# Kernel tuning notes

Measured on AMD Instinct MI355X. Metric: run time of the kernel, lower is better.

Reference implementation:

```python
import jax, jax.numpy as jnp
import numpy as np

N_ITER = 3
N_CLASS = 10
N_ROUTE = 1152  # 32*6*6

def _conv(x, w, b, stride):
    y = jax.lax.conv_general_dilated(x, w, window_strides=(stride, stride), padding='VALID',
                                     dimension_numbers=('NCHW', 'OIHW', 'NCHW'))
    return y + b[None, :, None, None]

def setup_inputs() -> dict:
    key = jax.random.key(0)
    ks = jax.random.split(key, 7)
    B = 256
    return {
        'x': jax.random.normal(ks[0], (B, 1, 28, 28), jnp.float32),
        'conv1_w': jax.random.normal(ks[1], (256, 1, 9, 9), jnp.float32) * 0.05,
        'conv1_b': jax.random.normal(ks[2], (256,), jnp.float32) * 0.05,
        'conv2_w': jax.random.normal(ks[3], (256, 256, 9, 9), jnp.float32) * 0.02,
        'conv2_b': jax.random.normal(ks[4], (256,), jnp.float32) * 0.02,
        'W': jax.random.normal(ks[5], (10, 32, 6, 6, 16, 8), jnp.float32) * 0.1,
        'Wb': jax.random.normal(ks[6], (10, 32, 6, 6, 16), jnp.float32) * 0.1,
    }

def reference(x, conv1_w, conv1_b, conv2_w, conv2_b, W, Wb):
    # conv1 (no activation, matching the original forward)
    h = _conv(x, conv1_w, conv1_b, 1)                 # [B,256,20,20]
    prim = _conv(h, conv2_w, conv2_b, 2)              # [B,256,6,6]
    prim = prim.reshape(-1, 32, 6, 6, 8)              # same raw .view as torch
    # fused per-location linear: u_hat[b,j,k,l,i,o]
    u_hat = jnp.einsum('bjklc,ijkloc->bjklio', prim, W) + Wb.transpose(1, 2, 3, 0, 4)[None]
    B = u_hat.shape[0]
    xr = u_hat.reshape(B, N_CLASS, N_ROUTE, 16)       # same raw .view as torch
    bij = jnp.zeros((N_CLASS, N_ROUTE), u_hat.dtype)
    v = None
    for r in range(N_ITER):
        c = jax.nn.softmax(bij, axis=1)               # [10,1152]
        v = jnp.einsum('in,bink->bik', c, xr)         # [B,10,16]
        # squash over the whole [B,16] tensor per class i (as in original x.norm())
        nrm = jnp.sqrt(jnp.sum(v * v, axis=(0, 2), keepdims=True))
        n2 = nrm * nrm
        v = (n2 / (1.0 + n2)) * (v / nrm)
        if r < N_ITER - 1:
            bij = bij + jnp.einsum('bink,bik->in', xr, v)
    # torch.stack(outputs) -> [10,B,16], then .view(-1,10,16)
    return jnp.transpose(v, (1, 0, 2)).reshape(-1, N_CLASS, 16)
```

## Files before the change

kernel.cpp:

```cpp
#include <hip/hip_runtime.h>
#include <hip/hip_bf16.h>

#define DI __device__ __forceinline__

typedef unsigned int u32;
typedef unsigned short u16;
typedef __attribute__((ext_vector_type(8))) short short8;
typedef __attribute__((ext_vector_type(4))) float f32x4;

DI u16 f2bf(float f) {
  union { float f; u32 x; } t; t.f = f;
  u32 x = t.x;
  u32 r = (x + 0x7fffu + ((x >> 16) & 1u)) >> 16;
  return (u16)r;
}

typedef __attribute__((address_space(3))) u32 lds_u32;
typedef const __attribute__((address_space(1))) u32 gbl_u32;
DI void gl_lds16(const u16* g, u16* l) {
  __builtin_amdgcn_global_load_lds((gbl_u32*)(const void*)g, (lds_u32*)(void*)l, 16, 0, 0);
}

__global__ __launch_bounds__(256) void pre_kernel(
    const float* __restrict__ x, const float* __restrict__ w1,
    const float* __restrict__ b1, const float* __restrict__ w2,
    u16* __restrict__ hT, u16* __restrict__ w2bT) {
  __shared__ union {
    struct { float xs[784]; u16 im[400 * 96]; u16 ws[256 * 96]; } c1;
    float w2s[5184];
  } S;
  int tid = threadIdx.x;
  if (blockIdx.x >= 256) {
    int oc = blockIdx.x - 256;
    for (int ch = 0; ch < 4; ++ch) {
      __syncthreads();
      for (int t = tid; t < 5184; t += 256) S.w2s[t] = w2[(size_t)oc * 20736 + ch * 5184 + t];
      __syncthreads();
      for (int t = tid; t < 5184; t += 256) {
        int tap = t >> 6, icl = t & 63;
        w2bT[((size_t)tap * 256 + oc) * 256 + ch * 64 + icl] = f2bf(S.w2s[icl * 81 + tap]);
      }
    }
    return;
  }
  int b = blockIdx.x;
  int lane = tid & 63, wid = tid >> 6;
  const float* xb = x + (size_t)b * 784;
  for (int t = tid; t < 784; t += 256) S.c1.xs[t] = xb[t];
  for (int t = tid; t < 20736; t += 256) {
    int oc = t / 81, kk = t % 81;
    int g = (kk >> 3) & 3, ph = (kk & ~31) | (((g ^ ((oc >> 1) & 3)) << 3)) | (kk & 7);
    S.c1.ws[oc * 96 + ph] = f2bf(w1[t]);
  }
  for (int t = tid; t < 256 * 15; t += 256) {
    int oc = t / 15, kk = 81 + t % 15;
    int g = (kk >> 3) & 3, ph = (kk & ~31) | (((g ^ ((oc >> 1) & 3)) << 3)) | (kk & 7);
    S.c1.ws[oc * 96 + ph] = 0;
  }
  __syncthreads();
  for (int t = tid; t < 32400; t += 256) {
    int pix = t / 81, kk = t % 81;
    int py = pix / 20, px = pix % 20, ky = kk / 9, kx = kk % 9;
    int g = (kk >> 3) & 3, ph = (kk & ~31) | (((g ^ ((pix >> 1) & 3)) << 3)) | (kk & 7);
    S.c1.im[pix * 96 + ph] = f2bf(S.c1.xs[(py + ky) * 28 + px + kx]);
  }
  for (int t = tid; t < 400 * 15; t += 256) {
    int pix = t / 15, kk = 81 + t % 15;
    int g = (kk >> 3) & 3, ph = (kk & ~31) | (((g ^ ((pix >> 1) & 3)) << 3)) | (kk & 7);
    S.c1.im[pix * 96 + ph] = 0;
  }
  __syncthreads();
  int l15 = lane & 15, lh = lane >> 4;
  int slot8 = (lh ^ ((l15 >> 1) & 3)) << 3;
  short8 br[4][3];
  float bias[4];
#pragma unroll
  for (int ni = 0; ni < 4; ++ni) {
    int row = wid * 64 + ni * 16 + l15;
    bias[ni] = b1[row];
#pragma unroll
    for (int ksb = 0; ksb < 3; ++ksb)
      br[ni][ksb] = *(const short8*)&S.c1.ws[row * 96 + ksb * 32 + slot8];
  }
  for (int mt = 0; mt < 25; ++mt) {
    f32x4 acc[4];
#pragma unroll
    for (int ni = 0; ni < 4; ++ni) acc[ni] = (f32x4){0.f, 0.f, 0.f, 0.f};
    short8 ar[3];
#pragma unroll
    for (int ksb = 0; ksb < 3; ++ksb)
      ar[ksb] = *(const short8*)&S.c1.im[(mt * 16 + l15) * 96 + ksb * 32 + slot8];
#pragma unroll
    for (int ksb = 0; ksb < 3; ++ksb)
#pragma unroll
      for (int ni = 0; ni < 4; ++ni)
        acc[ni] = __builtin_amdgcn_mfma_f32_16x16x32_bf16(ar[ksb], br[ni][ksb], acc[ni], 0, 0, 0);
#pragma unroll
    for (int ni = 0; ni < 4; ++ni)
#pragma unroll
      for (int reg = 0; reg < 4; ++reg)
        hT[((size_t)b * 400 + mt * 16 + lh * 4 + reg) * 256 + wid * 64 + ni * 16 + l15] =
            f2bf(acc[ni][reg] + bias[ni]);
  }
}

__global__ __launch_bounds__(512, 2) void conv2_mfma_kernel(
    const u16* __restrict__ hT, const u16* __restrict__ w2bT,
    float* __restrict__ pp) {
  __shared__ u16 Ab[2][16384];
  __shared__ u16 Bb[2][16384];
  int bid = blockIdx.x;
  int xcd = bid & 7, rank = bid >> 3;
  int work = (xcd < 4 ? xcd * 32 : 128 + (xcd - 4) * 31) + rank;
  int ks = work / 36, p = work % 36;
  int py = p / 6, px = p % 6;
  int tid = threadIdx.x, wid = tid >> 6, lane = tid & 63;
  int ntap = (ks < 4) ? 12 : 11;
  int nch = ntap * 4;

  const u16* srcA[4];
  const u16* srcB[4];
#pragma unroll
  for (int c = 0; c < 4; ++c) {
    int row = wid * 32 + c * 8 + (lane >> 3);
    int gsw = ((lane & 7) ^ (row & 7)) * 8;
    srcA[c] = hT + (size_t)row * 102400 + gsw;
    srcB[c] = w2bT + (size_t)row * 256 + gsw;
  }

  f32x4 acc[8][4];
#pragma unroll
  for (int i = 0; i < 8; ++i)
#pragma unroll
    for (int j = 0; j < 4; ++j) acc[i][j] = (f32x4){0.f, 0.f, 0.f, 0.f};

  int wr = wid >> 2, wc = wid & 3;
  int l15 = lane & 15, lh = lane >> 4;

  {
    int tap = ks;
    int pix = (2 * py + tap / 9) * 20 + (2 * px + tap % 9);
    int tofsA = pix * 256;
    size_t tofsB = (size_t)tap * 65536;
#pragma unroll
    for (int c = 0; c < 4; ++c) {
      gl_lds16(srcA[c] + tofsA, &Ab[0][(wid * 32 + c * 8) * 64]);
      gl_lds16(srcB[c] + tofsB, &Bb[0][(wid * 32 + c * 8) * 64]);
    }
  }

  for (int ch = 0; ch < nch; ++ch) {
    __syncthreads();
    int buf = ch & 1;
    if (ch + 1 < nch) {
      int nc2 = ch + 1;
      int tap = (nc2 >> 2) * 7 + ks;
      int icc = nc2 & 3;
      int pix = (2 * py + tap / 9) * 20 + (2 * px + tap % 9);
      int tofsA = pix * 256 + icc * 64;
      size_t tofsB = (size_t)tap * 65536 + icc * 64;
#pragma unroll
      for (int c = 0; c < 4; ++c) {
        gl_lds16(srcA[c] + tofsA, &Ab[buf ^ 1][(wid * 32 + c * 8) * 64]);
        gl_lds16(srcB[c] + tofsB, &Bb[buf ^ 1][(wid * 32 + c * 8) * 64]);
      }
    }
#pragma unroll
    for (int kk = 0; kk < 2; ++kk) {
      int g = kk * 4 + lh;
      short8 br[4];
#pragma unroll
      for (int ni = 0; ni < 4; ++ni) {
        int row = wc * 64 + ni * 16 + l15;
        br[ni] = *(const short8*)&Bb[buf][row * 64 + ((g ^ (row & 7)) * 8)];
      }
#pragma unroll
      for (int mi = 0; mi < 8; ++mi) {
        int row = wr * 128 + mi * 16 + l15;
        short8 ar = *(const short8*)&Ab[buf][row * 64 + ((g ^ (row & 7)) * 8)];
#pragma unroll
        for (int ni = 0; ni < 4; ++ni)
          acc[mi][ni] = __builtin_amdgcn_mfma_f32_16x16x32_bf16(ar, br[ni], acc[mi][ni], 0, 0, 0);
      }
    }
  }

  float* ppk = pp + (size_t)ks * 2359296 + (size_t)p * 256;
#pragma unroll
  for (int mi = 0; mi < 8; ++mi) {
    int b = wr * 128 + mi * 16 + lh * 4;
#pragma unroll
    for (int ni = 0; ni < 4; ++ni) {
      int oc = wc * 64 + ni * 16 + l15;
      *(float4*)&ppk[(size_t)oc * 9216 + b] = *(float4*)&acc[mi][ni];
    }
  }
}

__global__ __launch_bounds__(256) void cwvgemm_kernel(
    const float* __restrict__ bij, const float* __restrict__ W,
    const float* __restrict__ Wb, const float* __restrict__ pp,
    const float* __restrict__ b2, float* __restrict__ prim2T,
    float* __restrict__ vp, float* __restrict__ cbp, int first) {
  __shared__ float cS[1152];
  __shared__ float cws[512];
  __shared__ float red[256];
  __shared__ float cbl[40][16];
  int ch = blockIdx.x, i = blockIdx.y, tid = threadIdx.x;
  if (first) {
    for (int n = tid; n < 1152; n += 256) cS[n] = 1.0f / 1152.0f;
  } else {
    const float* brow = bij + i * 1152;
    float m = -1e30f;
    for (int n = tid; n < 1152; n += 256) m = fmaxf(m, brow[n]);
    red[tid] = m; __syncthreads();
    for (int s = 128; s > 0; s >>= 1) { if (tid < s) red[tid] = fmaxf(red[tid], red[tid + s]); __syncthreads(); }
    m = red[0]; __syncthreads();
    float sum = 0.f;
    for (int n = tid; n < 1152; n += 256) sum += expf(brow[n] - m);
    red[tid] = sum; __syncthreads();
    for (int s = 128; s > 0; s >>= 1) { if (tid < s) red[tid] += red[tid + s]; __syncthreads(); }
    float inv = 1.0f / red[0];
    for (int n = tid; n < 1152; n += 256) cS[n] = expf(brow[n] - m) * inv;
  }
  __syncthreads();
  int loc_min = (i * 1152) / 10, loc_max = ((i + 1) * 1152 - 1) / 10;
  int lc0 = loc_min + ch * 4;
  for (int t = tid; t < 512; t += 256) {
    int ll = t >> 7, rem = t & 127, k = rem >> 3, cc = rem & 7;
    int loc = lc0 + ll;
    float a = 0.f;
    if (loc <= loc_max) {
      for (int io = 0; io < 10; ++io) {
        int mm = loc * 10 + io;
        if (mm / 1152 == i)
          a += cS[mm - i * 1152] * W[(size_t)io * 147456 + (size_t)loc * 128 + k * 8 + cc];
      }
    }
    cws[ll * 128 + cc * 16 + k] = a;
  }
  if (tid < 40) {
    int ll = tid / 10, io = tid % 10;
    int loc = lc0 + ll;
    float cv = 0.f;
    if (loc <= loc_max) {
      int mm = loc * 10 + io;
      if (mm / 1152 == i) cv = cS[mm - i * 1152];
    }
    if (cv != 0.f) {
      const float* wb = Wb + (size_t)io * 18432 + (size_t)loc * 16;
#pragma unroll
      for (int k = 0; k < 16; ++k) cbl[tid][k] = cv * wb[k];
    } else {
#pragma unroll
      for (int k = 0; k < 16; ++k) cbl[tid][k] = 0.f;
    }
  }
  __syncthreads();
  if (tid < 16) {
    float s = 0.f;
    for (int q = 0; q < 40; ++q) s += cbl[q][tid];
    cbp[(size_t)(ch * 10 + i) * 16 + tid] = s;
  }
  float acc[16];
#pragma unroll
  for (int k = 0; k < 16; ++k) acc[k] = 0.f;
  for (int ll = 0; ll < 4; ++ll) {
    int loc = lc0 + ll;
    if (loc > loc_max) break;
    const float* cw = cws + ll * 128;
#pragma unroll
    for (int cc = 0; cc < 8; ++cc) {
      int flat = loc * 8 + cc;
      float pvv;
      if (first) {
        pvv = b2[flat / 36];
#pragma unroll
        for (int ks = 0; ks < 7; ++ks)
          pvv += pp[(size_t)ks * 2359296 + (size_t)flat * 256 + tid];
        prim2T[(size_t)flat * 256 + tid] = pvv;
      } else {
        pvv = prim2T[(size_t)flat * 256 + tid];
      }
      float4 a0 = *(const float4*)&cw[cc * 16];
      float4 a1 = *(const float4*)&cw[cc * 16 + 4];
      float4 a2 = *(const float4*)&cw[cc * 16 + 8];
      float4 a3 = *(const float4*)&cw[cc * 16 + 12];
      acc[0] += pvv * a0.x; acc[1] += pvv * a0.y; acc[2] += pvv * a0.z; acc[3] += pvv * a0.w;
      acc[4] += pvv * a1.x; acc[5] += pvv * a1.y; acc[6] += pvv * a1.z; acc[7] += pvv * a1.w;
      acc[8] += pvv * a2.x; acc[9] += pvv * a2.y; acc[10] += pvv * a2.z; acc[11] += pvv * a2.w;
      acc[12] += pvv * a3.x; acc[13] += pvv * a3.y; acc[14] += pvv * a3.z; acc[15] += pvv * a3.w;
    }
  }
  float* dst = vp + ((size_t)(ch * 10 + i) * 256 + tid) * 16;
#pragma unroll
  for (int k = 0; k < 16; ++k) dst[k] = acc[k];
}

__global__ __launch_bounds__(256) void vred_kernel(
    const float* __restrict__ vp, const float* __restrict__ cbp,
    float* __restrict__ vpre, float* __restrict__ ssp, float* __restrict__ svp) {
  __shared__ float red[256];
  __shared__ float sh[16][17];
  int bs = blockIdx.x, i = blockIdx.y, tid = threadIdx.x;
  int bl = tid >> 4, k = tid & 15;
  int b = bs * 16 + bl;
  float a = 0.f;
  for (int ch = 0; ch < 32; ++ch) a += vp[((size_t)(ch * 10 + i) * 256 + b) * 16 + k];
  float cb = 0.f;
  for (int ch = 0; ch < 32; ++ch) cb += cbp[(size_t)(ch * 10 + i) * 16 + k];
  a += cb;
  vpre[((size_t)i * 256 + b) * 16 + k] = a;
  red[tid] = a * a;
  sh[bl][k] = a;
  __syncthreads();
  for (int s = 128; s > 0; s >>= 1) { if (tid < s) red[tid] += red[tid + s]; __syncthreads(); }
  for (int s = 8; s > 0; s >>= 1) { if (bl < s) sh[bl][k] += sh[bl + s][k]; __syncthreads(); }
  if (tid == 0) ssp[i * 16 + bs] = red[0];
  if (tid < 16) svp[(size_t)(i * 16 + bs) * 16 + tid] = sh[0][tid];
}

__global__ __launch_bounds__(256) void pv_bij_kernel(
    const float* __restrict__ vpre, const float* __restrict__ ssp,
    const float* __restrict__ svp, const float* __restrict__ prim2T,
    const float* __restrict__ W, const float* __restrict__ Wb,
    float* __restrict__ bij, int first) {
  __shared__ float ps[32 * 260];
  __shared__ float vs[2 * 16 * 260];
  __shared__ float Ps[32][32];
  __shared__ float scl[2];
  __shared__ float svl[2][16];
  int blk = blockIdx.x, tid = threadIdx.x;
  int loc0 = blk * 4;
  int I = (loc0 * 10) / 1152;
  if (tid < 2) {
    int cls = I + tid;
    float ss = 0.f;
    if (cls <= 9)
      for (int q = 0; q < 16; ++q) ss += ssp[cls * 16 + q];
    float nrm = sqrtf(ss);
    scl[tid] = (cls <= 9 && nrm > 0.f) ? nrm / (1.f + nrm * nrm) : 0.f;
  }
  if (tid < 32) {
    int cl = tid >> 4, k = tid & 15;
    int cls = I + cl;
    float s = 0.f;
    if (cls <= 9)
      for (int q = 0; q < 16; ++q) s += svp[(size_t)(cls * 16 + q) * 16 + k];
    svl[cl][k] = s;
  }
  for (int t = tid; t < 2048; t += 256) {
    int row = t >> 6, seg = t & 63;
    float4 a = *(const float4*)(prim2T + (size_t)(loc0 * 8 + row) * 256 + seg * 4);
    *(float4*)&ps[row * 260 + seg * 4] = a;
  }
  __syncthreads();
  for (int cl = 0; cl < 2; ++cl) {
    int cls = I + cl;
    float sc = scl[cl];
    for (int t = tid; t < 4096; t += 256) {
      int b = t >> 4, k = t & 15;
      float val = (cls <= 9) ? vpre[(size_t)cls * 4096 + t] * sc : 0.f;
      vs[(cl * 16 + k) * 260 + b] = val;
    }
  }
  __syncthreads();
  {
    int k = tid & 15, fs = tid >> 4;
    const float4* ps4 = (const float4*)ps;
    const float4* vs4 = (const float4*)vs;
#pragma unroll
    for (int q = 0; q < 4; ++q) {
      int flat_l = fs * 2 + (q & 1);
      int slot = q >> 1;
      int loc = loc0 + (flat_l >> 3);
      int cls = (loc * 10) / 1152 + slot;
      int cl_idx = cls - I;
      if (cl_idx <= 1 && cls <= 9) {
        float a = 0.f;
        int bp = flat_l * 65, bv = (cl_idx * 16 + k) * 65;
        for (int b4 = 0; b4 < 64; ++b4) {
          float4 p4 = ps4[bp + b4];
          float4 w4 = vs4[bv + b4];
          a += p4.x * w4.x + p4.y * w4.y + p4.z * w4.z + p4.w * w4.w;
        }
        Ps[flat_l][slot * 16 + k] = a;
      }
    }
  }
  __syncthreads();
  if (tid < 40) {
    int ll = tid / 10, io = tid % 10;
    int loc = loc0 + ll;
    int m = loc * 10 + io;
    int i = m / 1152;
    int slot = i - (loc * 10) / 1152;
    int cl = i - I;
    const float* wrow = W + (size_t)io * 147456 + (size_t)loc * 128;
    float s = 0.f;
#pragma unroll
    for (int k = 0; k < 16; ++k) {
      float4 w0 = *(const float4*)(wrow + k * 8);
      float4 w1 = *(const float4*)(wrow + k * 8 + 4);
      s += w0.x * Ps[ll * 8 + 0][slot * 16 + k] + w0.y * Ps[ll * 8 + 1][slot * 16 + k]
         + w0.z * Ps[ll * 8 + 2][slot * 16 + k] + w0.w * Ps[ll * 8 + 3][slot * 16 + k];
      s += w1.x * Ps[ll * 8 + 4][slot * 16 + k] + w1.y * Ps[ll * 8 + 5][slot * 16 + k]
         + w1.z * Ps[ll * 8 + 6][slot * 16 + k] + w1.w * Ps[ll * 8 + 7][slot * 16 + k];
    }
    const float* wbr = Wb + (size_t)io * 18432 + (size_t)loc * 16;
    float scsv = scl[cl];
#pragma unroll
    for (int k = 0; k < 16; ++k) s += wbr[k] * (scsv * svl[cl][k]);
    bij[m] = first ? s : (bij[m] + s);
  }
}

__global__ __launch_bounds__(256) void outw_kernel(
    const float* __restrict__ vpre, const float* __restrict__ ssp,
    float* __restrict__ out) {
  int i = blockIdx.x, tid = threadIdx.x;
  float ss = 0.f;
  for (int q = 0; q < 16; ++q) ss += ssp[i * 16 + q];
  float nrm = sqrtf(ss);
  float scale = (nrm > 0.f) ? nrm / (1.f + nrm * nrm) : 0.f;
  for (int t = tid; t < 4096; t += 256)
    out[(size_t)i * 4096 + t] = vpre[(size_t)i * 4096 + t] * scale;
}

extern "C" void kernel_launch(void* const* d_in, const int* in_sizes, int n_in,
                              void* d_out, int out_size, void* d_ws, size_t ws_size,
                              hipStream_t stream) {
  const float* x  = (const float*)d_in[0];
  const float* w1 = (const float*)d_in[1];
  const float* b1 = (const float*)d_in[2];
  const float* w2 = (const float*)d_in[3];
  const float* b2 = (const float*)d_in[4];
  const float* W  = (const float*)d_in[5];
  const float* Wb = (const float*)d_in[6];
  float* out = (float*)d_out;

  u16*   hT     = (u16*)d_ws;
  u16*   w2bT   = hT + 26214400;
  float* pp     = (float*)(w2bT + 5308416);
  float* prim2T = pp + 7 * 2359296;
  float* vp     = prim2T + 2359296;
  float* vpre   = vp + 1310720;
  float* bij    = vpre + 40960;
  float* ssp    = bij + 11520;
  float* svp    = ssp + 160;
  float* cbp    = svp + 2560;

  pre_kernel<<<512, 256, 0, stream>>>(x, w1, b1, w2, hT, w2bT);
  conv2_mfma_kernel<<<252, 512, 0, stream>>>(hT, w2bT, pp);

  for (int r = 0; r < 3; ++r) {
    cwvgemm_kernel<<<dim3(32, 10), 256, 0, stream>>>(bij, W, Wb, pp, b2, prim2T, vp, cbp,
                                                     r == 0 ? 1 : 0);
    vred_kernel<<<dim3(16, 10), 256, 0, stream>>>(vp, cbp, vpre, ssp, svp);
    if (r < 2) {
      pv_bij_kernel<<<288, 256, 0, stream>>>(vpre, ssp, svp, prim2T, W, Wb, bij,
                                             r == 0 ? 1 : 0);
    } else {
      outw_kernel<<<10, 256, 0, stream>>>(vpre, ssp, out);
    }
  }
}
```

Before: 304.1 us.

## Triple-buffer conv2 LDS pipeline with finer K chunks and explicit vmcnt waits

The conv2 GEMM kernel moves from a double-buffered 64-wide K chunk to a triple-buffered 32-wide chunk. Loads are issued two stages ahead, with explicit s_waitcnt vmcnt and raw s_barrier instead of __syncthreads, and s_setprio is raised around the MFMA block. The aim is to hide global-to-LDS latency and cut barrier stalls, at the cost of twice as many iterations and a new swizzle layout. Separately, the conv1 pre-kernel converts the input to bf16 once and builds im2col per pixel with an unrolled loop, avoiding per-element div/mod.

Measured after the change: 308.0 us. Within noise of the previous version (+1.3%).

```diff
diff --git a/kernel.cpp b/kernel.cpp
--- a/kernel.cpp
+++ b/kernel.cpp
@@ -26,7 +26,7 @@
     const float* __restrict__ b1, const float* __restrict__ w2,
     u16* __restrict__ hT, u16* __restrict__ w2bT) {
   __shared__ union {
-    struct { float xs[784]; u16 im[400 * 96]; u16 ws[256 * 96]; } c1;
+    struct { u16 xbf[784]; u16 im[400 * 96]; u16 ws[256 * 96]; } c1;
     float w2s[5184];
   } S;
   int tid = threadIdx.x;
@@ -46,28 +46,36 @@
   int b = blockIdx.x;
   int lane = tid & 63, wid = tid >> 6;
   const float* xb = x + (size_t)b * 784;
-  for (int t = tid; t < 784; t += 256) S.c1.xs[t] = xb[t];
+  for (int t = tid; t < 784; t += 256) S.c1.xbf[t] = f2bf(xb[t]);
   for (int t = tid; t < 20736; t += 256) {
     int oc = t / 81, kk = t % 81;
-    int g = (kk >> 3) & 3, ph = (kk & ~31) | (((g ^ ((oc >> 1) & 3)) << 3)) | (kk & 7);
+    int g = (kk >> 3) & 3, ph = (kk & 96) | (((g ^ ((oc >> 1) & 3)) << 3)) | (kk & 7);
     S.c1.ws[oc * 96 + ph] = f2bf(w1[t]);
   }
   for (int t = tid; t < 256 * 15; t += 256) {
     int oc = t / 15, kk = 81 + t % 15;
-    int g = (kk >> 3) & 3, ph = (kk & ~31) | (((g ^ ((oc >> 1) & 3)) << 3)) | (kk & 7);
+    int g = (kk >> 3) & 3, ph = (kk & 96) | (((g ^ ((oc >> 1) & 3)) << 3)) | (kk & 7);
     S.c1.ws[oc * 96 + ph] = 0;
   }
   __syncthreads();
-  for (int t = tid; t < 32400; t += 256) {
-    int pix = t / 81, kk = t % 81;
-    int py = pix / 20, px = pix % 20, ky = kk / 9, kx = kk % 9;
-    int g = (kk >> 3) & 3, ph = (kk & ~31) | (((g ^ ((pix >> 1) & 3)) << 3)) | (kk & 7);
-    S.c1.im[pix * 96 + ph] = f2bf(S.c1.xs[(py + ky) * 28 + px + kx]);
-  }
-  for (int t = tid; t < 400 * 15; t += 256) {
-    int pix = t / 15, kk = 81 + t % 15;
-    int g = (kk >> 3) & 3, ph = (kk & ~31) | (((g ^ ((pix >> 1) & 3)) << 3)) | (kk & 7);
-    S.c1.im[pix * 96 + ph] = 0;
+  for (int pix = tid; pix < 400; pix += 256) {
+    int py = pix / 20, px = pix - py * 20;
+    int c2 = (pix >> 1) & 3;
+    u16* dst = &S.c1.im[pix * 96];
+    const u16* src = &S.c1.xbf[py * 28 + px];
+#pragma unroll
+    for (int ky = 0; ky < 9; ++ky)
+#pragma unroll
+      for (int kx = 0; kx < 9; ++kx) {
+        int kk = ky * 9 + kx;
+        int ph = (kk & 96) | ((((kk >> 3) & 3) ^ c2) << 3) | (kk & 7);
+        dst[ph] = src[ky * 28 + kx];
+      }
+#pragma unroll
+    for (int kk = 81; kk < 96; ++kk) {
+      int ph = (kk & 96) | ((((kk >> 3) & 3) ^ c2) << 3) | (kk & 7);
+      dst[ph] = 0;
+    }
   }
   __syncthreads();
   int l15 = lane & 15, lh = lane >> 4;
@@ -107,8 +115,8 @@
 __global__ __launch_bounds__(512, 2) void conv2_mfma_kernel(
     const u16* __restrict__ hT, const u16* __restrict__ w2bT,
     float* __restrict__ pp) {
-  __shared__ u16 Ab[2][16384];
-  __shared__ u16 Bb[2][16384];
+  __shared__ u16 Ab[3 * 8192];
+  __shared__ u16 Bb[3 * 8192];
   int bid = blockIdx.x;
   int xcd = bid & 7, rank = bid >> 3;
   int work = (xcd < 4 ? xcd * 32 : 128 + (xcd - 4) * 31) + rank;
@@ -116,17 +124,28 @@
   int py = p / 6, px = p % 6;
   int tid = threadIdx.x, wid = tid >> 6, lane = tid & 63;
   int ntap = (ks < 4) ? 12 : 11;
-  int nch = ntap * 4;
-
-  const u16* srcA[4];
-  const u16* srcB[4];
-#pragma unroll
-  for (int c = 0; c < 4; ++c) {
-    int row = wid * 32 + c * 8 + (lane >> 3);
-    int gsw = ((lane & 7) ^ (row & 7)) * 8;
-    srcA[c] = hT + (size_t)row * 102400 + gsw;
-    srcB[c] = w2bT + (size_t)row * 256 + gsw;
-  }
+  int nch = ntap * 8;
+
+  int gsw = ((tid & 3) ^ ((tid >> 3) & 3)) * 8;
+  int srow = tid >> 2;
+  const u16* baseA0 = hT + (size_t)srow * 102400 + gsw;
+  const u16* baseA1 = hT + (size_t)(128 + srow) * 102400 + gsw;
+  const u16* baseB0 = w2bT + (size_t)srow * 256 + gsw;
+  const u16* baseB1 = w2bT + (size_t)(128 + srow) * 256 + gsw;
+
+#define STAGE(T, BUF) do {                                          \
+    int tap_ = ((T) >> 3) * 7 + ks;                                 \
+    int icc_ = ((T) & 7) << 5;                                      \
+    int pix_ = (2 * py + tap_ / 9) * 20 + (2 * px + tap_ % 9);      \
+    int tofsA_ = pix_ * 256 + icc_;                                 \
+    size_t tofsB_ = (size_t)tap_ * 65536 + icc_;                    \
+    u16* la_ = &Ab[(BUF) * 8192 + tid * 8];                         \
+    u16* lb_ = &Bb[(BUF) * 8192 + tid * 8];                         \
+    gl_lds16(baseA0 + tofsA_, la_);                                 \
+    gl_lds16(baseA1 + tofsA_, la_ + 4096);                          \
+    gl_lds16(baseB0 + tofsB_, lb_);                                 \
+    gl_lds16(baseB1 + tofsB_, lb_ + 4096);                          \
+  } while (0)
 
   f32x4 acc[8][4];
 #pragma unroll
@@ -137,53 +156,45 @@
   int wr = wid >> 2, wc = wid & 3;
   int l15 = lane & 15, lh = lane >> 4;
 
-  {
-    int tap = ks;
-    int pix = (2 * py + tap / 9) * 20 + (2 * px + tap % 9);
-    int tofsA = pix * 256;
-    size_t tofsB = (size_t)tap * 65536;
-#pragma unroll
-    for (int c = 0; c < 4; ++c) {
-      gl_lds16(srcA[c] + tofsA, &Ab[0][(wid * 32 + c * 8) * 64]);
-      gl_lds16(srcB[c] + tofsB, &Bb[0][(wid * 32 + c * 8) * 64]);
-    }
-  }
-
-  for (int ch = 0; ch < nch; ++ch) {
-    __syncthreads();
-    int buf = ch & 1;
-    if (ch + 1 < nch) {
-      int nc2 = ch + 1;
-      int tap = (nc2 >> 2) * 7 + ks;
-      int icc = nc2 & 3;
-      int pix = (2 * py + tap / 9) * 20 + (2 * px + tap % 9);
-      int tofsA = pix * 256 + icc * 64;
-      size_t tofsB = (size_t)tap * 65536 + icc * 64;
-#pragma unroll
-      for (int c = 0; c < 4; ++c) {
-        gl_lds16(srcA[c] + tofsA, &Ab[buf ^ 1][(wid * 32 + c * 8) * 64]);
-        gl_lds16(srcB[c] + tofsB, &Bb[buf ^ 1][(wid * 32 + c * 8) * 64]);
-      }
-    }
-#pragma unroll
-    for (int kk = 0; kk < 2; ++kk) {
-      int g = kk * 4 + lh;
-      short8 br[4];
-#pragma unroll
-      for (int ni = 0; ni < 4; ++ni) {
-        int row = wc * 64 + ni * 16 + l15;
-        br[ni] = *(const short8*)&Bb[buf][row * 64 + ((g ^ (row & 7)) * 8)];
-      }
-#pragma unroll
-      for (int mi = 0; mi < 8; ++mi) {
-        int row = wr * 128 + mi * 16 + l15;
-        short8 ar = *(const short8*)&Ab[buf][row * 64 + ((g ^ (row & 7)) * 8)];
-#pragma unroll
-        for (int ni = 0; ni < 4; ++ni)
-          acc[mi][ni] = __builtin_amdgcn_mfma_f32_16x16x32_bf16(ar, br[ni], acc[mi][ni], 0, 0, 0);
-      }
-    }
-  }
+  STAGE(0, 0);
+  STAGE(1, 1);
+
+  int bufR = 0;
+  for (int t = 0; t < nch; ++t) {
+    if (t + 2 < nch) {
+      int bufS = (bufR == 0) ? 2 : bufR - 1;
+      STAGE(t + 2, bufS);
+      asm volatile("s_waitcnt vmcnt(8)" ::: "memory");
+    } else if (t + 1 < nch) {
+      asm volatile("s_waitcnt vmcnt(4)" ::: "memory");
+    } else {
+      asm volatile("s_waitcnt vmcnt(0)" ::: "memory");
+    }
+    asm volatile("s_barrier" ::: "memory");
+    const u16* A = &Ab[bufR * 8192];
+    const u16* B = &Bb[bufR * 8192];
+    short8 ar[8], br[4];
+#pragma unroll
+    for (int ni = 0; ni < 4; ++ni) {
+      int row = wc * 64 + ni * 16 + l15;
+      br[ni] = *(const short8*)&B[row * 32 + ((lh ^ ((row >> 1) & 3)) * 8)];
+    }
+#pragma unroll
+    for (int mi = 0; mi < 8; ++mi) {
+      int row = wr * 128 + mi * 16 + l15;
+      ar[mi] = *(const short8*)&A[row * 32 + ((lh ^ ((row >> 1) & 3)) * 8)];
+    }
+    __builtin_amdgcn_s_setprio(1);
+#pragma unroll
+    for (int mi = 0; mi < 8; ++mi)
+#pragma unroll
+      for (int ni = 0; ni < 4; ++ni)
+        acc[mi][ni] = __builtin_amdgcn_mfma_f32_16x16x32_bf16(ar[mi], br[ni], acc[mi][ni], 0, 0, 0);
+    __builtin_amdgcn_s_setprio(0);
+    asm volatile("s_barrier" ::: "memory");
+    bufR = (bufR == 2) ? 0 : bufR + 1;
+  }
+#undef STAGE
 
   float* ppk = pp + (size_t)ks * 2359296 + (size_t)p * 256;
 #pragma unroll
```
